# Optimization experiments

Hardware: AMD Instinct MI355X
Metric: run time of the kernel (lower is better)

## Reference

```python
import jax, jax.numpy as jnp
import numpy as np

BOHR = 0.5291772105638411   # Angstrom per Bohr (ase.units.Bohr)
HA = 27.211386024367243     # eV per Hartree (ase.units.Ha)
S6, S8, A1, A2 = 1.0, 0.7875, 0.4289, 4.4407
CN_ONSET, CN_CUTOFF = 20.0, 25.0
E2_ONSET, E2_CUTOFF = 55.0, 60.0
KCN = 16.0   # exponent of ncoord.exp_count
WF = 4.0     # gaussian_weight factor

N_ATOMS = 100000
N_EDGES = 3200000
N_ELEM = 95
N_REF = 5


def smooth_cutoff(dr, r_onset, r_cutoff):
    """HOOMD-style C^1 multiplicative isotropic cutoff S(dr)."""
    r_c = jnp.float32(r_cutoff) ** jnp.float32(2)
    r_o = jnp.float32(r_onset) ** jnp.float32(2)
    r = dr ** jnp.float32(2)
    inner = jnp.where(
        dr < r_cutoff,
        (r_c - r) ** 2 * (r_c + 2 * r - 3 * r_o) / (r_c - r_o) ** 3,
        0.0,
    )
    return jnp.where(dr < r_onset, 1.0, inner)


def setup_inputs() -> dict:
    key = jax.random.key(0)
    k1, k2, k3, k4, k5, k6, k7 = jax.random.split(key, 7)
    dr_vec = jax.random.normal(k1, (N_EDGES, 3), dtype=jnp.float32)
    ref_cn_table = jax.random.uniform(k2, (N_ELEM, N_REF), dtype=jnp.float32)
    ref_c6_table = jax.random.uniform(k3, (N_ELEM, N_ELEM, N_REF, N_REF), dtype=jnp.float32)
    r4r2_table = jax.random.uniform(k4, (N_ELEM,), dtype=jnp.float32) + 0.5
    rcov_table = jax.random.uniform(k5, (N_ELEM,), dtype=jnp.float32) + 0.5
    numbers = jax.random.randint(k6, (N_ATOMS,), 0, N_ELEM, dtype=jnp.int32)
    idx = jax.random.randint(k7, (2, N_EDGES), 0, N_ATOMS, dtype=jnp.int32)
    return {
        "dr_vec": dr_vec,
        "ref_cn_table": ref_cn_table,
        "ref_c6_table": ref_c6_table,
        "r4r2_table": r4r2_table,
        "rcov_table": rcov_table,
        "numbers": numbers,
        "idx": idx,
    }


def reference(dr_vec, ref_cn_table, ref_c6_table, r4r2_table, rcov_table, numbers, idx):
    n_atoms = numbers.shape[0]
    # per-edge distance, Angstrom -> Bohr
    dr = jnp.sqrt(jnp.sum(dr_vec * dr_vec, axis=-1)) / jnp.float32(BOHR)  # [E]
    i, j = idx[0], idx[1]
    Zi, Zj = numbers[i], numbers[j]

    # per-edge element data (D3Data.from_idxs)
    rc = rcov_table[Zi] + rcov_table[Zj]            # [E]
    qq = 3.0 * r4r2_table[Zi] * r4r2_table[Zj]      # [E]

    # coordination numbers: exp_count with smooth cutoff, segment-summed per atom
    count = 1.0 / (1.0 + jnp.exp(-KCN * (rc / dr - 1.0)))
    masked_cn = jnp.where(dr > 0, smooth_cutoff(dr, CN_ONSET, CN_CUTOFF) * count, 0.0)
    cn = jax.ops.segment_sum(masked_cn, i, num_segments=n_atoms)  # [N]

    # reference weights (gaussian weighting, normalized)
    ref_cn = ref_cn_table[numbers]                  # [N, R]
    dcn = ref_cn - cn[:, None]
    w = jnp.where(ref_cn >= 0, jnp.exp(-WF * dcn * dcn), 0.0)
    weights = w / (jnp.sum(w, -1, keepdims=True) + jnp.finfo(cn.dtype).eps)  # [N, R]

    # atomic C6 per edge
    ref_c6 = ref_c6_table[Zj, Zi]                   # [E, R, R]
    gw2 = weights[i][:, None, :] * weights[j][:, :, None]  # [E, R, R]
    c6 = jnp.sum(gw2 * ref_c6, axis=(-1, -2))       # [E]

    # rational (Becke-Johnson) damped two-body dispersion energy
    rr = A1 * jnp.sqrt(qq) + A2
    dr2 = dr * dr
    dr6 = dr2 * dr2 * dr2
    dr8 = dr6 * dr2
    rr2 = rr * rr
    rr6 = rr2 * rr2 * rr2
    rr8 = rr6 * rr2
    damped = -c6 * (S6 / (dr6 + rr6) + S8 * qq / (dr8 + rr8))
    energy = smooth_cutoff(dr, E2_ONSET, E2_CUTOFF) * damped / 2.0
    return jnp.sum(energy) * jnp.float32(HA)
```

## Files before the change

kernel.cpp:

```cpp
#include <hip/hip_runtime.h>
#include <hip/hip_fp16.h>

#define BOHR_F 0.5291772105638411f
#define HA_D   27.211386024367243
#define A1_F   0.4289f
#define A2_F   4.4407f
#define S6_F   1.0f
#define S8_F   0.7875f
#define KCN_F  16.0f
#define WF_F   4.0f
#define EPS_F  1.1920929e-07f

#define Q15_SCALE 32767.0f
#define Q15_INV   (1.0f/32767.0f)
#define DR_SCALE  512.0f
#define DR_INV    (1.0f/512.0f)
#define CN_SCALE 8388608.0f
#define CN_INV   (1.0f/8388608.0f)

#define NELEM  95
#define NBLK   512
#define BSW    512

__device__ __forceinline__ float smooth_cutoff(float dr, float r_on, float r_cut) {
    float r_c = r_cut * r_cut;
    float r_o = r_on * r_on;
    float r   = dr * dr;
    float den = (r_c - r_o);
    float t   = r_c - r;
    float inner = (dr < r_cut)
        ? (t * t * (r_c + 2.0f * r - 3.0f * r_o)) / (den * den * den)
        : 0.0f;
    return (dr < r_on) ? 1.0f : inner;
}

__device__ __forceinline__ float edge_m(float dr, float rc) {
    if (!(dr > 0.0f)) return 0.0f;
    float count = 1.0f / (1.0f + expf(-KCN_F * (rc / dr - 1.0f)));
    return smooth_cutoff(dr, 20.0f, 25.0f) * count;
}

__device__ __forceinline__ void u2f2(unsigned u, float& a, float& b) {
    __half2 h = __builtin_bit_cast(__half2, u);
    float2 f = __half22float2(h);
    a = f.x; b = f.y;
}

__device__ __forceinline__ int zfromR(uint4 R) {
    float z, dum;
    u2f2(R.w, z, dum);
    return (int)z;
}

__device__ __forceinline__ float edge_e8(float dr, uint4 Ri, uint4 Rj,
                                         uint4 c0, uint4 c1) {
    float wi[5], wj[5], qi, qj;
    u2f2(Ri.x, wi[0], wi[1]); u2f2(Ri.y, wi[2], wi[3]); u2f2(Ri.z, wi[4], qi);
    u2f2(Rj.x, wj[0], wj[1]); u2f2(Rj.y, wj[2], wj[3]); u2f2(Rj.z, wj[4], qj);
    unsigned w[7] = { c0.x, c0.y, c0.z, c0.w, c1.x, c1.y, c1.z };
    float sc = __uint_as_float(c1.w);
    float c6q = 0.0f;
#pragma unroll
    for (int a = 0; a < 5; ++a) {
#pragma unroll
        for (int b = 0; b < 5; ++b) {
            const int k = a * 5 + b;
            float qv = (float)((w[k >> 2] >> ((k & 3) * 8)) & 0xFFu);
            c6q += wj[a] * wi[b] * qv;
        }
    }
    float c6 = c6q * sc;
    float qq = 3.0f * qi * qj;
    float rr = A1_F * sqrtf(qq) + A2_F;
    float dr2 = dr * dr;
    float dr6 = dr2 * dr2 * dr2;
    float dr8 = dr6 * dr2;
    float rr2 = rr * rr;
    float rr6 = rr2 * rr2 * rr2;
    float rr8 = rr6 * rr2;
    float damped = -c6 * (S6_F / (dr6 + rr6) + S8_F * qq / (dr8 + rr8));
    return smooth_cutoff(dr, 55.0f, 60.0f) * damped * 0.5f;
}

__global__ __launch_bounds__(256)
void k_prep_c6u8(const float* __restrict__ src, unsigned char* __restrict__ dst,
                 int nrows) {
    int r = blockIdx.x * blockDim.x + threadIdx.x;
    if (r >= nrows) return;
    const float* s = src + (size_t)r * 25;
    float mx = 0.0f;
#pragma unroll
    for (int k = 0; k < 25; ++k) mx = fmaxf(mx, fabsf(s[k]));
    float sc  = mx * (1.0f / 255.0f);
    float inv = (mx > 0.0f) ? 255.0f / mx : 0.0f;
    unsigned w[8];
#pragma unroll
    for (int v = 0; v < 7; ++v) {
        unsigned acc = 0;
#pragma unroll
        for (int b = 0; b < 4; ++b) {
            int k = v * 4 + b;
            unsigned q = 0;
            if (k < 25) {
                float t = s[k] * inv;
                t = fmaxf(t, 0.0f);
                q = (unsigned)(t + 0.5f);
                if (q > 255u) q = 255u;
            }
            acc |= q << (b * 8);
        }
        w[v] = acc;
    }
    w[7] = __float_as_uint(sc);
    uint4* d = reinterpret_cast<uint4*>(dst + (size_t)r * 32);
    d[0] = make_uint4(w[0], w[1], w[2], w[3]);
    d[1] = make_uint4(w[4], w[5], w[6], w[7]);
}

__global__ __launch_bounds__(256)
void k_prep_atom(const int* __restrict__ numbers, const float* __restrict__ rcov,
                 uint2* __restrict__ rcovZ, int n_atoms) {
    int a = blockIdx.x * blockDim.x + threadIdx.x;
    if (a >= n_atoms) return;
    int Z = numbers[a];
    rcovZ[a] = make_uint2(__float_as_uint(rcov[Z]), (unsigned)Z);
}

__global__ __launch_bounds__(BSW, 4)
void k_hist(const int* __restrict__ idx_i, unsigned* __restrict__ ghist,
            int n_edges, int nb) {
    __shared__ unsigned hist[256];
    if (threadIdx.x < 256) hist[threadIdx.x] = 0;
    __syncthreads();
    int nquad = n_edges >> 2;
    int tid = blockIdx.x * blockDim.x + threadIdx.x;
    int stride = gridDim.x * blockDim.x;
    for (int qd = tid; qd < nquad; qd += stride) {
        int4 i4 = *reinterpret_cast<const int4*>(idx_i + (qd << 2));
        atomicAdd(&hist[i4.x >> 9], 1u);
        atomicAdd(&hist[i4.y >> 9], 1u);
        atomicAdd(&hist[i4.z >> 9], 1u);
        atomicAdd(&hist[i4.w >> 9], 1u);
    }
    for (int e = (nquad << 2) + tid; e < n_edges; e += stride)
        atomicAdd(&hist[idx_i[e] >> 9], 1u);
    __syncthreads();
    if ((int)threadIdx.x < nb)
        ghist[(size_t)threadIdx.x * gridDim.x + blockIdx.x] = hist[threadIdx.x];
}

__global__ __launch_bounds__(NBLK)
void k_scan_bucket(unsigned* __restrict__ ghist, unsigned* __restrict__ totals) {
    __shared__ unsigned s[NBLK];
    int b = blockIdx.x;
    int t = threadIdx.x;
    unsigned v = ghist[(size_t)b * NBLK + t];
    s[t] = v;
    __syncthreads();
    for (int off = 1; off < NBLK; off <<= 1) {
        unsigned x = (t >= off) ? s[t - off] : 0u;
        __syncthreads();
        s[t] += x;
        __syncthreads();
    }
    ghist[(size_t)b * NBLK + t] = s[t] - v;
    if (t == NBLK - 1) totals[b] = s[t];
}

__global__ __launch_bounds__(256)
void k_scan_base(const unsigned* __restrict__ totals,
                 unsigned* __restrict__ base, int nb) {
    __shared__ unsigned s[256];
    int t = threadIdx.x;
    unsigned v = (t < nb) ? totals[t] : 0u;
    s[t] = v;
    __syncthreads();
    for (int off = 1; off < 256; off <<= 1) {
        unsigned x = (t >= off) ? s[t - off] : 0u;
        __syncthreads();
        s[t] += x;
        __syncthreads();
    }
    if (t < nb) base[t] = s[t] - v;
    if (t == 255) base[nb] = s[t];
}

__global__ __launch_bounds__(BSW, 4)
void k_scatter_full(const float* __restrict__ dr_vec,
                    const int* __restrict__ idx_i,
                    const int* __restrict__ idx_j,
                    const uint2* __restrict__ rcovZ,
                    const unsigned* __restrict__ ghist,
                    const unsigned* __restrict__ base,
                    uint2* __restrict__ pairs,
                    int n_edges, int nb) {
    __shared__ unsigned ofs[256];
    if ((int)threadIdx.x < nb)
        ofs[threadIdx.x] = base[threadIdx.x]
                         + ghist[(size_t)threadIdx.x * gridDim.x + blockIdx.x];
    __syncthreads();
    int nquad = n_edges >> 2;
    int tid = blockIdx.x * blockDim.x + threadIdx.x;
    int stride = gridDim.x * blockDim.x;
    for (int qd = tid; qd < nquad; qd += stride) {
        int e0 = qd << 2;
        float4 v0 = *reinterpret_cast<const float4*>(dr_vec + 3 * e0);
        float4 v1 = *reinterpret_cast<const float4*>(dr_vec + 3 * e0 + 4);
        float4 v2 = *reinterpret_cast<const float4*>(dr_vec + 3 * e0 + 8);
        float drq[4];
        drq[0] = sqrtf(v0.x*v0.x + v0.y*v0.y + v0.z*v0.z) / BOHR_F;
        drq[1] = sqrtf(v0.w*v0.w + v1.x*v1.x + v1.y*v1.y) / BOHR_F;
        drq[2] = sqrtf(v1.z*v1.z + v1.w*v1.w + v2.x*v2.x) / BOHR_F;
        drq[3] = sqrtf(v2.y*v2.y + v2.z*v2.z + v2.w*v2.w) / BOHR_F;
        int4 i4 = *reinterpret_cast<const int4*>(idx_i + e0);
        int4 j4 = *reinterpret_cast<const int4*>(idx_j + e0);
        int ia[4] = { i4.x, i4.y, i4.z, i4.w };
        int ja[4] = { j4.x, j4.y, j4.z, j4.w };
        uint2 RiZ[4], RjZ[4];
#pragma unroll
        for (int k = 0; k < 4; ++k) { RiZ[k] = rcovZ[ia[k]]; RjZ[k] = rcovZ[ja[k]]; }
#pragma unroll
        for (int k = 0; k < 4; ++k) {
            float rc = __uint_as_float(RiZ[k].x) + __uint_as_float(RjZ[k].x);
            float m = edge_m(drq[k], rc);
            unsigned q = (unsigned)(m * Q15_SCALE + 0.5f);
            if (q > 0x7FFFu) q = 0x7FFFu;
            unsigned dq = (unsigned)(drq[k] * DR_SCALE + 0.5f);
            if (dq > 0x7FFFu) dq = 0x7FFFu;
            unsigned w0 = ((unsigned)ia[k] << 15) | q;
            unsigned w1 = ((unsigned)ja[k] << 15) | dq;
            unsigned pos = atomicAdd(&ofs[ia[k] >> 9], 1u);
            pairs[pos] = make_uint2(w0, w1);
        }
    }
    for (int e = (nquad << 2) + tid; e < n_edges; e += stride) {
        float x = dr_vec[3*e], y = dr_vec[3*e+1], z = dr_vec[3*e+2];
        float dr = sqrtf(x*x + y*y + z*z) / BOHR_F;
        int i = idx_i[e], j = idx_j[e];
        uint2 RiZ = rcovZ[i], RjZ = rcovZ[j];
        float m = edge_m(dr, __uint_as_float(RiZ.x) + __uint_as_float(RjZ.x));
        unsigned q = (unsigned)(m * Q15_SCALE + 0.5f);
        if (q > 0x7FFFu) q = 0x7FFFu;
        unsigned dq = (unsigned)(dr * DR_SCALE + 0.5f);
        if (dq > 0x7FFFu) dq = 0x7FFFu;
        unsigned pos = atomicAdd(&ofs[i >> 9], 1u);
        pairs[pos] = make_uint2(((unsigned)i << 15) | q,
                                ((unsigned)j << 15) | dq);
    }
}

__global__ __launch_bounds__(512)
void k_reduce_weights(const uint2* __restrict__ pairs,
                      const unsigned* __restrict__ base,
                      const int* __restrict__ numbers,
                      const float* __restrict__ ref_cn_table,
                      const float* __restrict__ r4r2,
                      __half* __restrict__ rec,
                      int n_atoms) {
    __shared__ unsigned hist[512];
    hist[threadIdx.x] = 0;
    __syncthreads();
    int b = blockIdx.x;
    unsigned start = base[b];
    unsigned end   = base[b + 1];
    for (unsigned k = start + threadIdx.x; k < end; k += 512) {
        unsigned p = pairs[k].x;
        atomicAdd(&hist[(p >> 15) & 511], p & 0x7FFFu);
    }
    __syncthreads();
    int a = (b << 9) + threadIdx.x;
    if (a < n_atoms) {
        float c = (float)hist[threadIdx.x] * Q15_INV;
        int Z = numbers[a];
        float w[5];
        float s = 0.0f;
#pragma unroll
        for (int r = 0; r < 5; ++r) {
            float rcn = ref_cn_table[Z * 5 + r];
            float d = rcn - c;
            float wv = (rcn >= 0.0f) ? expf(-WF_F * d * d) : 0.0f;
            w[r] = wv;
            s += wv;
        }
        float den = s + EPS_F;
        __half* rr = rec + (size_t)a * 8;
#pragma unroll
        for (int r = 0; r < 5; ++r) rr[r] = __float2half(w[r] / den);
        rr[5] = __float2half(r4r2[Z]);
        rr[6] = __float2half((float)Z);
        rr[7] = __float2half(0.0f);
    }
}

#define LOADC8(p, z) do { \
    const uint4* _cp = reinterpret_cast<const uint4*>(c6q + (size_t)(z) * 32); \
    p##0 = _cp[0]; p##1 = _cp[1]; } while (0)

__global__ __launch_bounds__(256, 1)
void k_energy_sorted(const uint2* __restrict__ pairs,
                     const __half* __restrict__ rec,
                     const unsigned char* __restrict__ c6q,
                     double* __restrict__ e_acc,
                     int n_edges) {
    double local = 0.0;
    const uint4* recv = reinterpret_cast<const uint4*>(rec);
    int nquad = n_edges >> 2;
    int tid = blockIdx.x * blockDim.x + threadIdx.x;
    int stride = gridDim.x * blockDim.x;
    for (int qd = tid; qd < nquad; qd += stride) {
        int e0 = qd << 2;
        uint4 pA = *reinterpret_cast<const uint4*>(pairs + e0);
        uint4 pB = *reinterpret_cast<const uint4*>(pairs + e0 + 2);
        unsigned i0 = pA.x >> 15, j0 = pA.y >> 15;
        unsigned i1 = pA.z >> 15, j1 = pA.w >> 15;
        unsigned i2 = pB.x >> 15, j2 = pB.y >> 15;
        unsigned i3 = pB.z >> 15, j3 = pB.w >> 15;
        float dr0 = (float)(pA.y & 0x7FFFu) * DR_INV;
        float dr1 = (float)(pA.w & 0x7FFFu) * DR_INV;
        float dr2 = (float)(pB.y & 0x7FFFu) * DR_INV;
        float dr3 = (float)(pB.w & 0x7FFFu) * DR_INV;
        uint4 Ri0 = recv[i0], Rj0 = recv[j0];
        uint4 Ri1 = recv[i1], Rj1 = recv[j1];
        uint4 Ri2 = recv[i2], Rj2 = recv[j2];
        uint4 Ri3 = recv[i3], Rj3 = recv[j3];
        int zp0 = zfromR(Rj0) * NELEM + zfromR(Ri0);
        int zp1 = zfromR(Rj1) * NELEM + zfromR(Ri1);
        int zp2 = zfromR(Rj2) * NELEM + zfromR(Ri2);
        int zp3 = zfromR(Rj3) * NELEM + zfromR(Ri3);
        uint4 a0, a1;   LOADC8(a, zp0);
        uint4 b0, b1;   LOADC8(b, zp1);
        uint4 c0, c1;   LOADC8(c, zp2);
        uint4 d0, d1;   LOADC8(d, zp3);
        local += (double)edge_e8(dr0, Ri0, Rj0, a0, a1);
        local += (double)edge_e8(dr1, Ri1, Rj1, b0, b1);
        local += (double)edge_e8(dr2, Ri2, Rj2, c0, c1);
        local += (double)edge_e8(dr3, Ri3, Rj3, d0, d1);
    }
    for (int e = (nquad << 2) + tid; e < n_edges; e += stride) {
        uint2 pr = pairs[e];
        unsigned i = pr.x >> 15;
        unsigned j = pr.y >> 15;
        float dr = (float)(pr.y & 0x7FFFu) * DR_INV;
        uint4 Ri = recv[i];
        uint4 Rj = recv[j];
        int zp = zfromR(Rj) * NELEM + zfromR(Ri);
        const uint4* cp = reinterpret_cast<const uint4*>(c6q + (size_t)zp * 32);
        local += (double)edge_e8(dr, Ri, Rj, cp[0], cp[1]);
    }

    __shared__ double sdata[4];
    for (int off = 32; off > 0; off >>= 1)
        local += __shfl_down(local, off, 64);
    int lane = threadIdx.x & 63;
    int wid  = threadIdx.x >> 6;
    if (lane == 0) sdata[wid] = local;
    __syncthreads();
    if (threadIdx.x == 0) {
        double s = sdata[0] + sdata[1] + sdata[2] + sdata[3];
        atomicAdd(e_acc, s);
    }
}

__global__ __launch_bounds__(256)
void k_edges_cn_atomic(const float* __restrict__ dr_vec,
                       const int* __restrict__ idx_i,
                       const int* __restrict__ idx_j,
                       const uint2* __restrict__ rcovZ,
                       unsigned* __restrict__ cn_u32,
                       int n_edges) {
    int e = blockIdx.x * blockDim.x + threadIdx.x;
    if (e >= n_edges) return;
    float x = dr_vec[3 * e + 0];
    float y = dr_vec[3 * e + 1];
    float z = dr_vec[3 * e + 2];
    float dr = sqrtf(x * x + y * y + z * z) / BOHR_F;
    int i = idx_i[e];
    int j = idx_j[e];
    uint2 RiZ = rcovZ[i], RjZ = rcovZ[j];
    float m = edge_m(dr, __uint_as_float(RiZ.x) + __uint_as_float(RjZ.x));
    unsigned q = (unsigned)(m * CN_SCALE + 0.5f);
    if (q) atomicAdd(&cn_u32[i], q);
}

__global__ __launch_bounds__(256)
void k_atom_weights_rec(const unsigned* __restrict__ cn_u32,
                        const int* __restrict__ numbers,
                        const float* __restrict__ ref_cn_table,
                        const float* __restrict__ r4r2,
                        __half* __restrict__ rec,
                        int n_atoms) {
    int a = blockIdx.x * blockDim.x + threadIdx.x;
    if (a >= n_atoms) return;
    float c = (float)cn_u32[a] * CN_INV;
    int Z = numbers[a];
    float w[5];
    float s = 0.0f;
#pragma unroll
    for (int r = 0; r < 5; ++r) {
        float rcn = ref_cn_table[Z * 5 + r];
        float d = rcn - c;
        float wv = (rcn >= 0.0f) ? expf(-WF_F * d * d) : 0.0f;
        w[r] = wv;
        s += wv;
    }
    float den = s + EPS_F;
    __half* rr = rec + (size_t)a * 8;
#pragma unroll
    for (int r = 0; r < 5; ++r) rr[r] = __float2half(w[r] / den);
    rr[5] = __float2half(r4r2[Z]);
    rr[6] = __float2half((float)Z);
    rr[7] = __float2half(0.0f);
}

__global__ __launch_bounds__(256)
void k_energy_unsorted(const float* __restrict__ dr_vec,
                       const int* __restrict__ idx_i,
                       const int* __restrict__ idx_j,
                       const __half* __restrict__ rec,
                       const unsigned char* __restrict__ c6q,
                       double* __restrict__ e_acc,
                       int n_edges) {
    double local = 0.0;
    const uint4* recv = reinterpret_cast<const uint4*>(rec);
    int tid = blockIdx.x * blockDim.x + threadIdx.x;
    int stride = gridDim.x * blockDim.x;
    for (int e = tid; e < n_edges; e += stride) {
        float x = dr_vec[3*e], y = dr_vec[3*e+1], z = dr_vec[3*e+2];
        float dr = sqrtf(x*x + y*y + z*z) / BOHR_F;
        int i = idx_i[e], j = idx_j[e];
        uint4 Ri = recv[i];
        uint4 Rj = recv[j];
        int zp = zfromR(Rj) * NELEM + zfromR(Ri);
        const uint4* cp = reinterpret_cast<const uint4*>(c6q + (size_t)zp * 32);
        local += (double)edge_e8(dr, Ri, Rj, cp[0], cp[1]);
    }
    __shared__ double sdata[4];
    for (int off = 32; off > 0; off >>= 1)
        local += __shfl_down(local, off, 64);
    int lane = threadIdx.x & 63;
    int wid  = threadIdx.x >> 6;
    if (lane == 0) sdata[wid] = local;
    __syncthreads();
    if (threadIdx.x == 0) {
        double s = sdata[0] + sdata[1] + sdata[2] + sdata[3];
        atomicAdd(e_acc, s);
    }
}

__global__ void k_finalize(const double* __restrict__ e_acc,
                           float* __restrict__ out) {
    out[0] = (float)(e_acc[0] * HA_D);
}

static inline size_t a16(size_t x) { return (x + 15) & ~(size_t)15; }

extern "C" void kernel_launch(void* const* d_in, const int* in_sizes, int n_in,
                              void* d_out, int out_size, void* d_ws, size_t ws_size,
                              hipStream_t stream) {
    const float* dr_vec      = (const float*)d_in[0];
    const float* ref_cn_tab  = (const float*)d_in[1];
    const float* ref_c6_tab  = (const float*)d_in[2];
    const float* r4r2        = (const float*)d_in[3];
    const float* rcov        = (const float*)d_in[4];
    const int*   numbers     = (const int*)d_in[5];
    const int*   idx         = (const int*)d_in[6];

    int n_atoms = in_sizes[5];
    int n_edges = in_sizes[6] / 2;
    const int* idx_i = idx;
    const int* idx_j = idx + n_edges;

    const int BS = 256;
    int nb = (n_atoms + 511) >> 9;
    int nrows = NELEM * NELEM;

    char* ws = (char*)d_ws;
    double* e_acc = (double*)ws;

    size_t off_rec = 16;
    size_t off_c6q = a16(off_rec + (size_t)n_atoms * 8 * 2);
    size_t off_rcZ = a16(off_c6q + (size_t)nrows * 32);
    size_t off_var = a16(off_rcZ + (size_t)n_atoms * 8);

    size_t s_pairs  = off_var;
    size_t s_ghist  = a16(s_pairs + (size_t)n_edges * 8);
    size_t s_tot    = a16(s_ghist + (size_t)nb * NBLK * 4);
    size_t s_base   = a16(s_tot + (size_t)nb * 4);
    size_t need_s   = s_base + (size_t)(nb + 1) * 4;

    size_t a_cn   = off_var;

    int grid_r  = (nrows + BS - 1) / BS;
    int grid_a  = (n_atoms + BS - 1) / BS;
    int nquad   = (n_edges + 3) >> 2;
    int grid_q  = (nquad + BS - 1) / BS;
    if (grid_q > 8192) grid_q = 8192;
    int grid_e1 = (n_edges + BS - 1) / BS;
    if (grid_e1 > 8192) grid_e1 = 8192;

    __half*        rec   = (__half*)(ws + off_rec);
    unsigned char* c6q   = (unsigned char*)(ws + off_c6q);
    uint2*         rcovZ = (uint2*)(ws + off_rcZ);

    k_prep_c6u8<<<grid_r, BS, 0, stream>>>(ref_c6_tab, c6q, nrows);
    k_prep_atom<<<grid_a, BS, 0, stream>>>(numbers, rcov, rcovZ, n_atoms);

    bool sortable = (n_atoms <= (1 << 17)) && (nb <= 256);

    if (sortable && ws_size >= need_s) {
        uint2*    pairs   = (uint2*)(ws + s_pairs);
        unsigned* ghist   = (unsigned*)(ws + s_ghist);
        unsigned* totals  = (unsigned*)(ws + s_tot);
        unsigned* base    = (unsigned*)(ws + s_base);

        hipMemsetAsync(d_ws, 0, 16, stream);

        k_hist<<<NBLK, BSW, 0, stream>>>(idx_i, ghist, n_edges, nb);
        k_scan_bucket<<<nb, NBLK, 0, stream>>>(ghist, totals);
        k_scan_base<<<1, 256, 0, stream>>>(totals, base, nb);
        k_scatter_full<<<NBLK, BSW, 0, stream>>>(dr_vec, idx_i, idx_j, rcovZ,
            ghist, base, pairs, n_edges, nb);
        k_reduce_weights<<<nb, 512, 0, stream>>>(pairs, base, numbers,
            ref_cn_tab, r4r2, rec, n_atoms);
        k_energy_sorted<<<grid_q, BS, 0, stream>>>(pairs, rec, c6q, e_acc,
                                                   n_edges);
    } else {
        unsigned* cn_u32 = (unsigned*)(ws + a_cn);
        hipMemsetAsync(d_ws, 0, 16, stream);
        hipMemsetAsync(cn_u32, 0, (size_t)n_atoms * 4, stream);

        int grid_e = (n_edges + BS - 1) / BS;
        k_edges_cn_atomic<<<grid_e, BS, 0, stream>>>(dr_vec, idx_i, idx_j,
            rcovZ, cn_u32, n_edges);
        k_atom_weights_rec<<<grid_a, BS, 0, stream>>>(cn_u32, numbers,
            ref_cn_tab, r4r2, rec, n_atoms);
        k_energy_unsorted<<<grid_e1, BS, 0, stream>>>(dr_vec, idx_i, idx_j,
            rec, c6q, e_acc, n_edges);
    }

    k_finalize<<<1, 1, 0, stream>>>(e_acc, (float*)d_out);
}
```

Measured before the change: 150.3 us.

## Precompute per-edge element-pair index at scatter and process eight edges per thread

```diff
diff --git a/kernel.cpp b/kernel.cpp
--- a/kernel.cpp
+++ b/kernel.cpp
@@ -44,12 +44,6 @@
     __half2 h = __builtin_bit_cast(__half2, u);
     float2 f = __half22float2(h);
     a = f.x; b = f.y;
-}
-
-__device__ __forceinline__ int zfromR(uint4 R) {
-    float z, dum;
-    u2f2(R.w, z, dum);
-    return (int)z;
 }
 
 __device__ __forceinline__ float edge_e8(float dr, uint4 Ri, uint4 Rj,
@@ -185,6 +179,7 @@
     if (t == 255) base[nb] = s[t];
 }
 
+template<bool ZS>
 __global__ __launch_bounds__(BSW, 4)
 void k_scatter_full(const float* __restrict__ dr_vec,
                     const int* __restrict__ idx_i,
@@ -193,6 +188,7 @@
                     const unsigned* __restrict__ ghist,
                     const unsigned* __restrict__ base,
                     uint2* __restrict__ pairs,
+                    unsigned short* __restrict__ zs,
                     int n_edges, int nb) {
     __shared__ unsigned ofs[256];
     if ((int)threadIdx.x < nb)
@@ -231,6 +227,7 @@
             unsigned w1 = ((unsigned)ja[k] << 15) | dq;
             unsigned pos = atomicAdd(&ofs[ia[k] >> 9], 1u);
             pairs[pos] = make_uint2(w0, w1);
+            if (ZS) zs[pos] = (unsigned short)(RjZ[k].y * NELEM + RiZ[k].y);
         }
     }
     for (int e = (nquad << 2) + tid; e < n_edges; e += stride) {
@@ -246,6 +243,7 @@
         unsigned pos = atomicAdd(&ofs[i >> 9], 1u);
         pairs[pos] = make_uint2(((unsigned)i << 15) | q,
                                 ((unsigned)j << 15) | dq);
+        if (ZS) zs[pos] = (unsigned short)(RjZ.y * NELEM + RiZ.y);
     }
 }
 
@@ -296,12 +294,105 @@
     const uint4* _cp = reinterpret_cast<const uint4*>(c6q + (size_t)(z) * 32); \
     p##0 = _cp[0]; p##1 = _cp[1]; } while (0)
 
+__global__ __launch_bounds__(256)
+void k_energy_sorted8(const uint2* __restrict__ pairs,
+                      const unsigned short* __restrict__ zs,
+                      const __half* __restrict__ rec,
+                      const unsigned char* __restrict__ c6q,
+                      double* __restrict__ e_acc,
+                      int n_edges) {
+    double local = 0.0;
+    const uint4* recv = reinterpret_cast<const uint4*>(rec);
+    int noct = n_edges >> 3;
+    int tid = blockIdx.x * blockDim.x + threadIdx.x;
+    int stride = gridDim.x * blockDim.x;
+    for (int oc = tid; oc < noct; oc += stride) {
+        int e0 = oc << 3;
+        const uint4* pp = reinterpret_cast<const uint4*>(pairs + e0);
+        uint4 p0 = pp[0], p1 = pp[1], p2 = pp[2], p3 = pp[3];
+        uint4 zv = *reinterpret_cast<const uint4*>(zs + e0);
+        unsigned iA = p0.x >> 15, jA = p0.y >> 15;
+        unsigned iB = p0.z >> 15, jB = p0.w >> 15;
+        unsigned iC = p1.x >> 15, jC = p1.y >> 15;
+        unsigned iD = p1.z >> 15, jD = p1.w >> 15;
+        unsigned iE = p2.x >> 15, jE = p2.y >> 15;
+        unsigned iF = p2.z >> 15, jF = p2.w >> 15;
+        unsigned iG = p3.x >> 15, jG = p3.y >> 15;
+        unsigned iH = p3.z >> 15, jH = p3.w >> 15;
+        float drA = (float)(p0.y & 0x7FFFu) * DR_INV;
+        float drB = (float)(p0.w & 0x7FFFu) * DR_INV;
+        float drC = (float)(p1.y & 0x7FFFu) * DR_INV;
+        float drD = (float)(p1.w & 0x7FFFu) * DR_INV;
+        float drE = (float)(p2.y & 0x7FFFu) * DR_INV;
+        float drF = (float)(p2.w & 0x7FFFu) * DR_INV;
+        float drG = (float)(p3.y & 0x7FFFu) * DR_INV;
+        float drH = (float)(p3.w & 0x7FFFu) * DR_INV;
+        int zpA = (int)(zv.x & 0xFFFFu), zpB = (int)(zv.x >> 16);
+        int zpC = (int)(zv.y & 0xFFFFu), zpD = (int)(zv.y >> 16);
+        int zpE = (int)(zv.z & 0xFFFFu), zpF = (int)(zv.z >> 16);
+        int zpG = (int)(zv.w & 0xFFFFu), zpH = (int)(zv.w >> 16);
+        uint4 cA0, cA1;  LOADC8(cA, zpA);
+        uint4 cB0, cB1;  LOADC8(cB, zpB);
+        uint4 cC0, cC1;  LOADC8(cC, zpC);
+        uint4 cD0, cD1;  LOADC8(cD, zpD);
+        uint4 cE0, cE1;  LOADC8(cE, zpE);
+        uint4 cF0, cF1;  LOADC8(cF, zpF);
+        uint4 cG0, cG1;  LOADC8(cG, zpG);
+        uint4 cH0, cH1;  LOADC8(cH, zpH);
+        uint4 RiA = recv[iA], RjA = recv[jA];
+        uint4 RiB = recv[iB], RjB = recv[jB];
+        uint4 RiC = recv[iC], RjC = recv[jC];
+        uint4 RiD = recv[iD], RjD = recv[jD];
+        uint4 RiE = recv[iE], RjE = recv[jE];
+        uint4 RiF = recv[iF], RjF = recv[jF];
+        uint4 RiG = recv[iG], RjG = recv[jG];
+        uint4 RiH = recv[iH], RjH = recv[jH];
+        local += (double)edge_e8(drA, RiA, RjA, cA0, cA1);
+        local += (double)edge_e8(drB, RiB, RjB, cB0, cB1);
+        local += (double)edge_e8(drC, RiC, RjC, cC0, cC1);
+        local += (double)edge_e8(drD, RiD, RjD, cD0, cD1);
+        local += (double)edge_e8(drE, RiE, RjE, cE0, cE1);
+        local += (double)edge_e8(drF, RiF, RjF, cF0, cF1);
+        local += (double)edge_e8(drG, RiG, RjG, cG0, cG1);
+        local += (double)edge_e8(drH, RiH, RjH, cH0, cH1);
+    }
+    for (int e = (noct << 3) + tid; e < n_edges; e += stride) {
+        uint2 pr = pairs[e];
+        unsigned i = pr.x >> 15;
+        unsigned j = pr.y >> 15;
+        float dr = (float)(pr.y & 0x7FFFu) * DR_INV;
+        uint4 Ri = recv[i];
+        uint4 Rj = recv[j];
+        int zp = (int)zs[e];
+        const uint4* cp = reinterpret_cast<const uint4*>(c6q + (size_t)zp * 32);
+        local += (double)edge_e8(dr, Ri, Rj, cp[0], cp[1]);
+    }
+
+    __shared__ double sdata[4];
+    for (int off = 32; off > 0; off >>= 1)
+        local += __shfl_down(local, off, 64);
+    int lane = threadIdx.x & 63;
+    int wid  = threadIdx.x >> 6;
+    if (lane == 0) sdata[wid] = local;
+    __syncthreads();
+    if (threadIdx.x == 0) {
+        double s = sdata[0] + sdata[1] + sdata[2] + sdata[3];
+        atomicAdd(e_acc, s);
+    }
+}
+
+__device__ __forceinline__ int zfromR(uint4 R) {
+    float z, dum;
+    u2f2(R.w, z, dum);
+    return (int)z;
+}
+
 __global__ __launch_bounds__(256, 1)
-void k_energy_sorted(const uint2* __restrict__ pairs,
-                     const __half* __restrict__ rec,
-                     const unsigned char* __restrict__ c6q,
-                     double* __restrict__ e_acc,
-                     int n_edges) {
+void k_energy_sorted4(const uint2* __restrict__ pairs,
+                      const __half* __restrict__ rec,
+                      const unsigned char* __restrict__ c6q,
+                      double* __restrict__ e_acc,
+                      int n_edges) {
     double local = 0.0;
     const uint4* recv = reinterpret_cast<const uint4*>(rec);
     int nquad = n_edges >> 2;
@@ -347,7 +438,6 @@
         const uint4* cp = reinterpret_cast<const uint4*>(c6q + (size_t)zp * 32);
         local += (double)edge_e8(dr, Ri, Rj, cp[0], cp[1]);
     }
-
     __shared__ double sdata[4];
     for (int off = 32; off > 0; off >>= 1)
         local += __shfl_down(local, off, 64);
@@ -482,16 +572,27 @@
     size_t off_rcZ = a16(off_c6q + (size_t)nrows * 32);
     size_t off_var = a16(off_rcZ + (size_t)n_atoms * 8);
 
-    size_t s_pairs  = off_var;
-    size_t s_ghist  = a16(s_pairs + (size_t)n_edges * 8);
-    size_t s_tot    = a16(s_ghist + (size_t)nb * NBLK * 4);
-    size_t s_base   = a16(s_tot + (size_t)nb * 4);
-    size_t need_s   = s_base + (size_t)(nb + 1) * 4;
-
-    size_t a_cn   = off_var;
+    size_t t1_pairs = off_var;
+    size_t t1_zs    = a16(t1_pairs + (size_t)n_edges * 8);
+    size_t t1_ghist = a16(t1_zs + (size_t)n_edges * 2);
+    size_t t1_tot   = a16(t1_ghist + (size_t)nb * NBLK * 4);
+    size_t t1_base  = a16(t1_tot + (size_t)nb * 4);
+    size_t need_t1  = t1_base + (size_t)(nb + 1) * 4;
+
+    size_t t2_pairs = off_var;
+    size_t t2_ghist = a16(t2_pairs + (size_t)n_edges * 8);
+    size_t t2_tot   = a16(t2_ghist + (size_t)nb * NBLK * 4);
+    size_t t2_base  = a16(t2_tot + (size_t)nb * 4);
+    size_t need_t2  = t2_base + (size_t)(nb + 1) * 4;
+
+    size_t a_cn = off_var;
 
     int grid_r  = (nrows + BS - 1) / BS;
     int grid_a  = (n_atoms + BS - 1) / BS;
+    int noct    = n_edges >> 3;
+    int grid_o  = (noct + BS - 1) / BS;
+    if (grid_o < 1) grid_o = 1;
+    if (grid_o > 8192) grid_o = 8192;
     int nquad   = (n_edges + 3) >> 2;
     int grid_q  = (nquad + BS - 1) / BS;
     if (grid_q > 8192) grid_q = 8192;
@@ -507,23 +608,33 @@
 
     bool sortable = (n_atoms <= (1 << 17)) && (nb <= 256);
 
-    if (sortable && ws_size >= need_s) {
-        uint2*    pairs   = (uint2*)(ws + s_pairs);
-        unsigned* ghist   = (unsigned*)(ws + s_ghist);
-        unsigned* totals  = (unsigned*)(ws + s_tot);
-        unsigned* base    = (unsigned*)(ws + s_base);
+    if (sortable && ws_size >= need_t2) {
+        bool zsOK = (ws_size >= need_t1);
+        uint2*          pairs  = (uint2*)(ws + (zsOK ? t1_pairs : t2_pairs));
+        unsigned short* zs     = zsOK ? (unsigned short*)(ws + t1_zs) : nullptr;
+        unsigned*       ghist  = (unsigned*)(ws + (zsOK ? t1_ghist : t2_ghist));
+        unsigned*       totals = (unsigned*)(ws + (zsOK ? t1_tot : t2_tot));
+        unsigned*       base   = (unsigned*)(ws + (zsOK ? t1_base : t2_base));
 
         hipMemsetAsync(d_ws, 0, 16, stream);
 
         k_hist<<<NBLK, BSW, 0, stream>>>(idx_i, ghist, n_edges, nb);
         k_scan_bucket<<<nb, NBLK, 0, stream>>>(ghist, totals);
         k_scan_base<<<1, 256, 0, stream>>>(totals, base, nb);
-        k_scatter_full<<<NBLK, BSW, 0, stream>>>(dr_vec, idx_i, idx_j, rcovZ,
-            ghist, base, pairs, n_edges, nb);
+        if (zsOK)
+            k_scatter_full<true><<<NBLK, BSW, 0, stream>>>(dr_vec, idx_i,
+                idx_j, rcovZ, ghist, base, pairs, zs, n_edges, nb);
+        else
+            k_scatter_full<false><<<NBLK, BSW, 0, stream>>>(dr_vec, idx_i,
+                idx_j, rcovZ, ghist, base, pairs, nullptr, n_edges, nb);
         k_reduce_weights<<<nb, 512, 0, stream>>>(pairs, base, numbers,
             ref_cn_tab, r4r2, rec, n_atoms);
-        k_energy_sorted<<<grid_q, BS, 0, stream>>>(pairs, rec, c6q, e_acc,
-                                                   n_edges);
+        if (zsOK)
+            k_energy_sorted8<<<grid_o, BS, 0, stream>>>(pairs, zs, rec, c6q,
+                e_acc, n_edges);
+        else
+            k_energy_sorted4<<<grid_q, BS, 0, stream>>>(pairs, rec, c6q,
+                e_acc, n_edges);
     } else {
         unsigned* cn_u32 = (unsigned*)(ws + a_cn);
         hipMemsetAsync(d_ws, 0, 16, stream);
```

Result: slower. 153.4 us (+2.0%).
